# Kernel tuning notes

Hardware: AMD Instinct MI355X
Metric: run time of the kernel (lower is better)

The kernel has to match this reference:

```python
import jax, jax.numpy as jnp
import numpy as np

S, B, D, T = 256, 64, 1024, 64
BOS, EOS, PAD = 0, 1, 2


def setup_inputs() -> dict:
    key = jax.random.key(0)
    k1, k2, k3, k4, k5 = jax.random.split(key, 5)
    features = jax.random.normal(k1, (S, B, D), jnp.float32)
    tags = jax.random.randint(k2, (S, B), 0, T)
    # valid lengths in [2, S] so the recurrence and gold gather are well-defined
    seq_lens = jax.random.randint(k3, (B,), 2, S + 1)
    W = jax.random.normal(k4, (T, D), jnp.float32) * 0.02  # feat2tag weight
    b = jnp.zeros((T,), jnp.float32)                        # feat2tag bias
    transitions = jax.random.normal(k5, (T, T), jnp.float32) * 0.01
    return {"features": features, "tags": tags, "seq_lens": seq_lens,
            "W": W, "b": b, "transitions": transitions}


def reference(features, tags, seq_lens, W, b, transitions):
    s_len, b_size = features.shape[0], features.shape[1]
    n_tags = transitions.shape[0]
    # crf_scores[t, b, i, j] = emit[t, b, i] + transitions[i, j]
    emit = jnp.einsum('sbd,td->sbt', features, W) + b        # (S,B,T)
    crf = emit[:, :, :, None] + transitions[None, None]      # (S,B,T,T)

    # ---- gold path score ----
    pad_row = jnp.full((1, b_size), PAD, tags.dtype)
    nxt_tags = jnp.concatenate([tags[1:], pad_row], axis=0)  # (S,B)
    flat_ix = tags * n_tags + nxt_tags                       # (S,B)
    step_sc = jnp.take_along_axis(
        crf.reshape(s_len, b_size, n_tags * n_tags),
        flat_ix[:, :, None], axis=2)[..., 0]                 # (S,B)
    cum = jnp.cumsum(step_sc, axis=0)                        # (S,B)
    gold = cum[seq_lens - 1, jnp.arange(b_size)].sum()

    # ---- partition function via masked forward recurrence (scan over time) ----
    cur0 = crf[0, :, BOS, :]                                 # (B,T)
    active = jnp.arange(1, s_len)[:, None] < seq_lens[None, :]  # (S-1,B)

    def step(cur, xs):
        crf_t, act = xs                                      # (B,T,T), (B,)
        # logsumexp over previous tag i: cur[b,i] + crf_t[b,i,j]
        nxt = jax.nn.logsumexp(cur[:, :, None] + crf_t, axis=1)  # (B,T)
        return jnp.where(act[:, None], nxt, cur), None

    cur, _ = jax.lax.scan(step, cur0, (crf[1:], active))
    return cur[:, EOS].sum() - gold
```

## Files before the change

### kernel.cpp

```cpp
#include <hip/hip_runtime.h>

#define SLEN 256
#define NB   64
#define ND   1024
#define NT   64
#define APAD 1032

typedef float f32x4  __attribute__((ext_vector_type(4)));
typedef short bf16x8 __attribute__((ext_vector_type(8)));
typedef __fp16 f16x8 __attribute__((ext_vector_type(8)));
typedef __fp16 f16x2 __attribute__((ext_vector_type(2)));
typedef unsigned int u32;
typedef u32 u32x2 __attribute__((ext_vector_type(2)));
typedef u32 u32x4 __attribute__((ext_vector_type(4)));
typedef int  i32x4 __attribute__((ext_vector_type(4)));

__device__ __forceinline__ u32 cvt_pk_bf16(float lo, float hi) {
  u32 r;
  asm("v_cvt_pk_bf16_f32 %0, %1, %2" : "=v"(r) : "v"(lo), "v"(hi));
  return r;
}

__device__ __forceinline__ u32 cvt_pk_f16(float lo, float hi) {
  union { f16x2 h; u32 u; } c;
  c.h = __builtin_amdgcn_cvt_pkrtz(lo, hi);
  return c.u;
}

__device__ __forceinline__ u32 pack_f16_rne(float lo, float hi) {
  union { _Float16 h[2]; u32 u; } c;
  c.h[0] = (_Float16)lo;
  c.h[1] = (_Float16)hi;
  return c.u;
}

__device__ __forceinline__ unsigned short f2bf(float f) {
  u32 u = __float_as_uint(f);
  return (unsigned short)((u + 0x7FFFu + ((u >> 16) & 1u)) >> 16);
}

__device__ __forceinline__ f32x4 vmax4(f32x4 a, f32x4 b) {
  f32x4 r;
  r.x = fmaxf(a.x, b.x); r.y = fmaxf(a.y, b.y);
  r.z = fmaxf(a.z, b.z); r.w = fmaxf(a.w, b.w);
  return r;
}

__global__ __launch_bounds__(256) void prep(const float* __restrict__ W,
                                            const float* __restrict__ trans,
                                            unsigned short* __restrict__ Wb3,
                                            u32* __restrict__ Ebuf,
                                            float* __restrict__ out) {
  if (blockIdx.x < 256) {
    int o  = blockIdx.x * 256 + threadIdx.x;
    int e  = o & 7;
    int l  = (o >> 3) & 63;
    int f  = (o >> 9) & 3;
    int k0 = o >> 11;
    int t  = f * 16 + (l & 15);
    int k  = k0 * 32 + ((l >> 4) << 3) + e;
    Wb3[o] = f2bf(W[t * ND + k]);
    return;
  }
  const int tid = threadIdx.x;
  if (tid == 0) out[0] = 0.f;
  const int l = tid & 63, wd = tid >> 6;
  const int q = l >> 4, c = l & 15;
#pragma unroll
  for (int mt = 0; mt < 4; ++mt)
#pragma unroll
    for (int kf = 0; kf < 2; ++kf) {
      float v0 = __expf(trans[(32 * kf + 8 * q + 2 * wd)     * NT + 16 * mt + c]) * 0.015625f;
      float v1 = __expf(trans[(32 * kf + 8 * q + 2 * wd + 1) * NT + 16 * mt + c]) * 0.015625f;
      Ebuf[(mt * 2 + kf) * 256 + l * 4 + wd] = pack_f16_rne(v0, v1);
    }
}

__global__ __launch_bounds__(256) void emit_gemm(const float* __restrict__ F,
                                                 const unsigned short* __restrict__ Wb3,
                                                 const float* __restrict__ bias,
                                                 unsigned short* __restrict__ xbuf) {
  __shared__ union ShU {
    unsigned short a[16 * APAD];
    float comb[4][64][17];
  } sh;
  const int tid = threadIdx.x;
  const int w   = tid >> 6;
  const int l   = tid & 63;
  const int q   = l >> 4;
  const int c   = l & 15;

  const int blk = blockIdx.x;
  const float* fb = F + (size_t)blk * 16 * ND;

#pragma unroll 8
  for (int i = 0; i < 16; ++i) {
    f32x4 v = *(const f32x4*)(fb + i * ND + tid * 4);
    u32x2 p;
    p.x = cvt_pk_bf16(v.x, v.y);
    p.y = cvt_pk_bf16(v.z, v.w);
    *(u32x2*)(sh.a + i * APAD + tid * 4) = p;
  }
  __syncthreads();

  f32x4 acc0 = {0.f, 0.f, 0.f, 0.f};
  f32x4 acc1 = acc0, acc2 = acc0, acc3 = acc0;
  const bf16x8* bptr = reinterpret_cast<const bf16x8*>(Wb3) + l;
  const unsigned short* arow = sh.a + c * APAD + q * 8;

#pragma unroll
  for (int g = 0; g < 8; ++g) {
    int ks = w * 8 + g;
    bf16x8 af = *(const bf16x8*)(arow + ks * 32);
    bf16x8 b0 = bptr[(ks * 4 + 0) * 64];
    bf16x8 b1 = bptr[(ks * 4 + 1) * 64];
    bf16x8 b2 = bptr[(ks * 4 + 2) * 64];
    bf16x8 b3 = bptr[(ks * 4 + 3) * 64];
    acc0 = __builtin_amdgcn_mfma_f32_16x16x32_bf16(af, b0, acc0, 0, 0, 0);
    acc1 = __builtin_amdgcn_mfma_f32_16x16x32_bf16(af, b1, acc1, 0, 0, 0);
    acc2 = __builtin_amdgcn_mfma_f32_16x16x32_bf16(af, b2, acc2, 0, 0, 0);
    acc3 = __builtin_amdgcn_mfma_f32_16x16x32_bf16(af, b3, acc3, 0, 0, 0);
  }

  __syncthreads();
#pragma unroll
  for (int r = 0; r < 4; ++r) {
    sh.comb[w][l][r]      = acc0[r];
    sh.comb[w][l][4 + r]  = acc1[r];
    sh.comb[w][l][8 + r]  = acc2[r];
    sh.comb[w][l][12 + r] = acc3[r];
  }
  __syncthreads();

  {
    float s[4];
#pragma unroll
    for (int r = 0; r < 4; ++r)
      s[r] = sh.comb[0][l][4 * w + r] + sh.comb[1][l][4 * w + r]
           + sh.comb[2][l][4 * w + r] + sh.comb[3][l][4 * w + r];
    const float bv = bias[16 * w + c];
    unsigned short* op = xbuf + (size_t)(blk * 16 + q * 4) * NT + 16 * w + c;
#pragma unroll
    for (int r = 0; r < 4; ++r)
      op[r * NT] = f2bf(__expf(s[r] + bv));
  }
}

__global__ __launch_bounds__(256, 2) void chunk_prod(
    const unsigned short* __restrict__ xbuf, const float* __restrict__ trans,
    const u32* __restrict__ Ebuf, const int* __restrict__ tags,
    const int* __restrict__ seq_lens, unsigned short* __restrict__ Gout,
    int* __restrict__ Gscale, float* __restrict__ Gpart) {
  __shared__ float trs[64 * 68];
  __shared__ unsigned short xlds[34 * 64];
  const int b   = blockIdx.x >> 3;
  const int k   = blockIdx.x & 7;
  const int tid = threadIdx.x;
  const int wid = tid >> 6;
  const int l   = tid & 63;
  const int q   = l >> 4, c = l & 15;

  const int L = seq_lens[b];

  {
    int tp  = tid >> 3;
    int cg  = (tid & 7) * 8;
    const u32x4* s4 = (const u32x4*)(xbuf + ((size_t)((32 * k + tp) * NB + b)) * NT + cg);
    *(u32x4*)(xlds + tp * 64 + cg) = *s4;
  }

  if (wid == 0) {
    float gp = 0.f;
    int s = 32 * k + (l & 31);
    if (l < 32 && s < L) {
      int tg = tags[s * NB + b];
      int nx = (s + 1 < SLEN) ? tags[(s + 1) * NB + b] : 2;
      float xv = __uint_as_float((u32)xbuf[(size_t)(s * NB + b) * NT + tg] << 16);
      gp = __logf(xv) + trans[tg * NT + nx];
    }
    gp += __shfl_xor(gp, 1, 64);
    gp += __shfl_xor(gp, 2, 64);
    gp += __shfl_xor(gp, 4, 64);
    gp += __shfl_xor(gp, 8, 64);
    gp += __shfl_xor(gp, 16, 64);
    if (l == 0) Gpart[b * 8 + k] = gp;
  }

  union uf { u32x4 u; f16x8 v; };
  uf ef[4][2];
#pragma unroll
  for (int mt = 0; mt < 4; ++mt)
#pragma unroll
    for (int kf = 0; kf < 2; ++kf)
      ef[mt][kf].u = *(const u32x4*)(Ebuf + (mt * 2 + kf) * 256 + l * 4);

  f32x4 g0 = {0,0,0,0}, g1 = g0, g2 = g0, g3 = g0;
  {
    int r = c - 4 * q;
    if (r >= 0 && r < 4) {
      float one = 1.0f;
      if (wid == 0) g0[r & 3] = one;
      else if (wid == 1) g1[r & 3] = one;
      else if (wid == 2) g2[r & 3] = one;
      else g3[r & 3] = one;
    }
  }

  int tbeg = 32 * k; if (tbeg < 1) tbeg = 1;
  int tend = 32 * k + 32; if (tend > L) tend = L;
  int exw = 0;

  __syncthreads();

#define SWAPQ(A, B) do {                                                  \
    asm("v_permlane32_swap_b32 %0, %1" : "+v"(A), "+v"(B));               \
    asm("v_permlane16_swap_b32 %0, %1" : "+v"(A), "+v"(B));               \
  } while (0)

#define LOADX(X, TP) do {                                                 \
    X[0] = *(const u32x2*)(xlds + (TP) * 64 + 4 * q);                     \
    X[1] = *(const u32x2*)(xlds + (TP) * 64 + 16 + 4 * q);                \
    X[2] = *(const u32x2*)(xlds + (TP) * 64 + 32 + 4 * q);                \
    X[3] = *(const u32x2*)(xlds + (TP) * 64 + 48 + 4 * q);                \
  } while (0)

#define MULPK(P0, P1, G, XW) do {                                         \
    f32x4 xv;                                                             \
    xv.x = __uint_as_float(XW.x << 16);                                   \
    xv.y = __uint_as_float(XW.x & 0xFFFF0000u);                           \
    xv.z = __uint_as_float(XW.y << 16);                                   \
    xv.w = __uint_as_float(XW.y & 0xFFFF0000u);                           \
    f32x4 ww = G * xv;                                                    \
    P0 = cvt_pk_f16(ww.x, ww.y);                                          \
    P1 = cvt_pk_f16(ww.z, ww.w);                                          \
  } while (0)

#define STEPF(X, T) do {                                                  \
    if ((((T) & 7) == 0) && ((T) != tbeg)) {         \
      f32x4 m4 = vmax4(vmax4(g0, g1), vmax4(g2, g3));                     \
      float mx = fmaxf(fmaxf(m4.x, m4.y), fmaxf(m4.z, m4.w));             \
      mx = fmaxf(mx, __shfl_xor(mx, 1, 64));                              \
      mx = fmaxf(mx, __shfl_xor(mx, 2, 64));                              \
      mx = fmaxf(mx, __shfl_xor(mx, 4, 64));                              \
      mx = fmaxf(mx, __shfl_xor(mx, 8, 64));                              \
      mx = fmaxf(mx, __shfl_xor(mx, 16, 64));                             \
      mx = fmaxf(mx, __shfl_xor(mx, 32, 64));                             \
      int ex = (int)((__float_as_uint(mx) >> 23) & 255u) - 127;           \
      float sc = __uint_as_float((u32)(127 - ex) << 23);                  \
      g0 *= sc; g1 *= sc; g2 *= sc; g3 *= sc; exw += ex;                  \
    }                                                                     \
    u32 p00, p01, p10, p11, p20, p21, p30, p31;                           \
    MULPK(p00, p01, g0, X[0]);                                            \
    MULPK(p10, p11, g1, X[1]);                                            \
    MULPK(p20, p21, g2, X[2]);                                            \
    MULPK(p30, p31, g3, X[3]);                                            \
    SWAPQ(p00, p10); SWAPQ(p01, p11); SWAPQ(p20, p30); SWAPQ(p21, p31);   \
    uf B0, B1;                                                            \
    B0.u[0] = p00; B0.u[1] = p01; B0.u[2] = p10; B0.u[3] = p11;           \
    B1.u[0] = p20; B1.u[1] = p21; B1.u[2] = p30; B1.u[3] = p31;           \
    const f32x4 zz = {0.f, 0.f, 0.f, 0.f};                                \
    g0 = __builtin_amdgcn_mfma_f32_16x16x32_f16(ef[0][0].v, B0.v, zz, 0, 0, 0); \
    g0 = __builtin_amdgcn_mfma_f32_16x16x32_f16(ef[0][1].v, B1.v, g0, 0, 0, 0); \
    g1 = __builtin_amdgcn_mfma_f32_16x16x32_f16(ef[1][0].v, B0.v, zz, 0, 0, 0); \
    g1 = __builtin_amdgcn_mfma_f32_16x16x32_f16(ef[1][1].v, B1.v, g1, 0, 0, 0); \
    g2 = __builtin_amdgcn_mfma_f32_16x16x32_f16(ef[2][0].v, B0.v, zz, 0, 0, 0); \
    g2 = __builtin_amdgcn_mfma_f32_16x16x32_f16(ef[2][1].v, B1.v, g2, 0, 0, 0); \
    g3 = __builtin_amdgcn_mfma_f32_16x16x32_f16(ef[3][0].v, B0.v, zz, 0, 0, 0); \
    g3 = __builtin_amdgcn_mfma_f32_16x16x32_f16(ef[3][1].v, B1.v, g3, 0, 0, 0); \
  } while (0)

  if (tbeg < tend) {
    u32x2 XA[4], XB[4];
    int tp  = tbeg - 32 * k;
    int tpe = tend - 32 * k;
    LOADX(XA, tp);
    for (; tp + 1 < tpe; tp += 2) {
      LOADX(XB, tp + 1);
      STEPF(XA, tp + 32 * k);
      LOADX(XA, tp + 2);
      STEPF(XB, tp + 1 + 32 * k);
    }
    if (tp < tpe) STEPF(XA, tp + 32 * k);
  }
#undef STEPF
#undef MULPK
#undef LOADX
#undef SWAPQ

  if (l == 0) Gscale[((size_t)b * 8 + k) * 4 + wid] = exw;

#pragma unroll
  for (int r = 0; r < 4; ++r) {
    trs[(4 * q + r) * 68      + 16 * wid + c] = g0[r];
    trs[(16 + 4 * q + r) * 68 + 16 * wid + c] = g1[r];
    trs[(32 + 4 * q + r) * 68 + 16 * wid + c] = g2[r];
    trs[(48 + 4 * q + r) * 68 + 16 * wid + c] = g3[r];
  }
  __syncthreads();
  {
    int row = tid >> 2, qt = tid & 3;
    const float* src = trs + row * 68 + qt * 16;
    u32 wp[8];
#pragma unroll
    for (int m = 0; m < 8; ++m) wp[m] = cvt_pk_bf16(src[2 * m], src[2 * m + 1]);
    u32x4* dst = (u32x4*)(Gout + (((size_t)(b * 8 + k) * 64 + row) * 64 + qt * 16));
    dst[0] = *(u32x4*)&wp[0];
    dst[1] = *(u32x4*)&wp[4];
  }
}

__global__ __launch_bounds__(64, 1) void chain_apply(
    const unsigned short* __restrict__ xbuf, const float* __restrict__ trans,
    const unsigned short* __restrict__ Gout, const int* __restrict__ Gscale,
    const float* __restrict__ Gpart, const int* __restrict__ seq_lens,
    float* __restrict__ out) {
  __shared__ __align__(16) float elds[64];
  const int b = blockIdx.x;
  const int j = threadIdx.x;
  const int L = seq_lens[b];

  float gp = (j < 8) ? Gpart[b * 8 + j] : 0.f;
  gp += __shfl_xor(gp, 1, 64);
  gp += __shfl_xor(gp, 2, 64);
  gp += __shfl_xor(gp, 4, 64);

  float A    = __expf(trans[j]);
  float logZ = __logf(__uint_as_float((u32)xbuf[(size_t)b * NT] << 16));

  const unsigned short* gbase = Gout + (size_t)b * 8 * 4096 + (size_t)j * 64;
  const i32x4* sbase = (const i32x4*)(Gscale + (size_t)b * 8 * 4);
  u32x4 gc[8], gn[8];
  i32x4 scc, scn;
#pragma unroll
  for (int m = 0; m < 8; ++m) gc[m] = *((const u32x4*)gbase + m);
  scc = sbase[0];

  const float C6 = 6.f * 0.6931471805599453f;

  for (int k = 0; k < 8; ++k) {
    if (k < 7) {
      const u32x4* gb2 = (const u32x4*)(gbase + (size_t)(k + 1) * 4096);
#pragma unroll
      for (int m = 0; m < 8; ++m) gn[m] = gb2[m];
      scn = sbase[k + 1];
    }
    int tb = 32 * k; if (tb < 1) tb = 1;
    int te = 32 * k + 32; if (te > L) te = L;
    int n = te - tb;
    if (n > 0) {
      elds[j] = A;
      float sA0 = 0.f, sA1 = 0.f, sA2 = 0.f, sA3 = 0.f;
      float sB0 = 0.f, sB1 = 0.f, sB2 = 0.f, sB3 = 0.f;
#pragma unroll
      for (int m = 0; m < 8; ++m) {
        f32x4 av0 = *(const f32x4*)(elds + 8 * m);
        f32x4 av1 = *(const f32x4*)(elds + 8 * m + 4);
        u32x4 w = gc[m];
        float a0, a1;
        a0 = fmaf(av0.x, __uint_as_float(w.x << 16),         0.f);
        a0 = fmaf(av0.y, __uint_as_float(w.x & 0xFFFF0000u), a0);
        a0 = fmaf(av0.z, __uint_as_float(w.y << 16),         a0);
        a0 = fmaf(av0.w, __uint_as_float(w.y & 0xFFFF0000u), a0);
        a1 = fmaf(av1.x, __uint_as_float(w.z << 16),         0.f);
        a1 = fmaf(av1.y, __uint_as_float(w.z & 0xFFFF0000u), a1);
        a1 = fmaf(av1.z, __uint_as_float(w.w << 16),         a1);
        a1 = fmaf(av1.w, __uint_as_float(w.w & 0xFFFF0000u), a1);
        switch (m >> 1) {
          case 0: if (m & 1) { sB0 += a0 + a1; } else { sA0 += a0 + a1; } break;
          case 1: if (m & 1) { sB1 += a0 + a1; } else { sA1 += a0 + a1; } break;
          case 2: if (m & 1) { sB2 += a0 + a1; } else { sA2 += a0 + a1; } break;
          default: if (m & 1) { sB3 += a0 + a1; } else { sA3 += a0 + a1; } break;
        }
      }
      float sc0 = __uint_as_float((u32)(127 + scc.x) << 23);
      float sc1 = __uint_as_float((u32)(127 + scc.y) << 23);
      float sc2 = __uint_as_float((u32)(127 + scc.z) << 23);
      float sc3 = __uint_as_float((u32)(127 + scc.w) << 23);
      A = ((sA0 + sB0) * sc0 + (sA1 + sB1) * sc1)
        + ((sA2 + sB2) * sc2 + (sA3 + sB3) * sc3);
      logZ += C6 * (float)n;
      u32 bb = __builtin_amdgcn_readfirstlane(__float_as_uint(A));
      int ex = (int)((bb >> 23) & 255u) - 127;
      A *= __uint_as_float((u32)(127 - ex) << 23);
      logZ += (float)ex * 0.6931471805599453f;
    }
    if (k < 7) {
#pragma unroll
      for (int m = 0; m < 8; ++m) gc[m] = gn[m];
      scc = scn;
    }
  }

  float res = logZ + __logf(A);
  res = __shfl(res, 1, 64);
  if (j == 0) atomicAdd(out, res - gp);
}

extern "C" void kernel_launch(void* const* d_in, const int* in_sizes, int n_in,
                              void* d_out, int out_size, void* d_ws, size_t ws_size,
                              hipStream_t stream) {
  const float* F     = (const float*)d_in[0];
  const int*   tags  = (const int*)  d_in[1];
  const int*   seq   = (const int*)  d_in[2];
  const float* W     = (const float*)d_in[3];
  const float* bias  = (const float*)d_in[4];
  const float* trans = (const float*)d_in[5];
  float* out = (float*)d_out;

  char* ws = (char*)d_ws;
  unsigned short* xbuf   = (unsigned short*)ws;
  unsigned short* Wb3    = (unsigned short*)(ws + 2228224);
  u32*            Ebuf   = (u32*)(ws + 2359296);
  unsigned short* Gout   = (unsigned short*)(ws + 2367488);
  int*            Gscale = (int*)(ws + 6561792);
  float*          Gpart  = (float*)(ws + 6569984);

  prep       <<<257,  256, 0, stream>>>(W, trans, Wb3, Ebuf, out);
  emit_gemm  <<<1024, 256, 0, stream>>>(F, Wb3, bias, xbuf);
  chunk_prod <<<512,  256, 0, stream>>>(xbuf, trans, Ebuf, tags, seq, Gout, Gscale, Gpart);
  chain_apply<<<64,    64, 0, stream>>>(xbuf, trans, Gout, Gscale, Gpart, seq, out);
}
```

Before: 45.70 us.

## Switch chunk products to split bf16 MFMA with 16-step chunks, drop rescaling

Replaces the f16 transition-matrix MFMA with a hi/lo bf16 split (two bf16 MFMAs per product, summed), which removes the periodic in-chunk max/rescale reduction and the per-chunk exponent array. Chunks shrink from 32 to 16 time steps, doubling the chunk_prod grid and raising the occupancy hint. In return the sequential chain_apply must apply 16 chunk matrices instead of 8, and the per-step MFMA count doubles. The loop is also simplified to a single step per iteration without software prefetch of the next step's LDS data.

After: 52.65 us. +15.2%, slower.

```diff
diff --git a/kernel.cpp b/kernel.cpp
--- a/kernel.cpp
+++ b/kernel.cpp
@@ -8,12 +8,9 @@
 
 typedef float f32x4  __attribute__((ext_vector_type(4)));
 typedef short bf16x8 __attribute__((ext_vector_type(8)));
-typedef __fp16 f16x8 __attribute__((ext_vector_type(8)));
-typedef __fp16 f16x2 __attribute__((ext_vector_type(2)));
 typedef unsigned int u32;
 typedef u32 u32x2 __attribute__((ext_vector_type(2)));
 typedef u32 u32x4 __attribute__((ext_vector_type(4)));
-typedef int  i32x4 __attribute__((ext_vector_type(4)));
 
 __device__ __forceinline__ u32 cvt_pk_bf16(float lo, float hi) {
   u32 r;
@@ -21,29 +18,9 @@
   return r;
 }
 
-__device__ __forceinline__ u32 cvt_pk_f16(float lo, float hi) {
-  union { f16x2 h; u32 u; } c;
-  c.h = __builtin_amdgcn_cvt_pkrtz(lo, hi);
-  return c.u;
-}
-
-__device__ __forceinline__ u32 pack_f16_rne(float lo, float hi) {
-  union { _Float16 h[2]; u32 u; } c;
-  c.h[0] = (_Float16)lo;
-  c.h[1] = (_Float16)hi;
-  return c.u;
-}
-
 __device__ __forceinline__ unsigned short f2bf(float f) {
   u32 u = __float_as_uint(f);
   return (unsigned short)((u + 0x7FFFu + ((u >> 16) & 1u)) >> 16);
-}
-
-__device__ __forceinline__ f32x4 vmax4(f32x4 a, f32x4 b) {
-  f32x4 r;
-  r.x = fmaxf(a.x, b.x); r.y = fmaxf(a.y, b.y);
-  r.z = fmaxf(a.z, b.z); r.w = fmaxf(a.w, b.w);
-  return r;
 }
 
 __global__ __launch_bounds__(256) void prep(const float* __restrict__ W,
@@ -72,7 +49,11 @@
     for (int kf = 0; kf < 2; ++kf) {
       float v0 = __expf(trans[(32 * kf + 8 * q + 2 * wd)     * NT + 16 * mt + c]) * 0.015625f;
       float v1 = __expf(trans[(32 * kf + 8 * q + 2 * wd + 1) * NT + 16 * mt + c]) * 0.015625f;
-      Ebuf[(mt * 2 + kf) * 256 + l * 4 + wd] = pack_f16_rne(v0, v1);
+      u32 u0 = __float_as_uint(v0), u1 = __float_as_uint(v1);
+      float h0 = __uint_as_float((u0 + 0x7FFFu + ((u0 >> 16) & 1u)) & 0xFFFF0000u);
+      float h1 = __uint_as_float((u1 + 0x7FFFu + ((u1 >> 16) & 1u)) & 0xFFFF0000u);
+      Ebuf[((mt * 2 + kf) * 2 + 0) * 256 + l * 4 + wd] = cvt_pk_bf16(h0, h1);
+      Ebuf[((mt * 2 + kf) * 2 + 1) * 256 + l * 4 + wd] = cvt_pk_bf16(v0 - h0, v1 - h1);
     }
 }
 
@@ -146,15 +127,15 @@
   }
 }
 
-__global__ __launch_bounds__(256, 2) void chunk_prod(
+__global__ __launch_bounds__(256, 4) void chunk_prod(
     const unsigned short* __restrict__ xbuf, const float* __restrict__ trans,
     const u32* __restrict__ Ebuf, const int* __restrict__ tags,
     const int* __restrict__ seq_lens, unsigned short* __restrict__ Gout,
-    int* __restrict__ Gscale, float* __restrict__ Gpart) {
+    float* __restrict__ Gpart) {
   __shared__ float trs[64 * 68];
-  __shared__ unsigned short xlds[34 * 64];
-  const int b   = blockIdx.x >> 3;
-  const int k   = blockIdx.x & 7;
+  __shared__ unsigned short xlds[16 * 64];
+  const int b   = blockIdx.x >> 4;
+  const int k   = blockIdx.x & 15;
   const int tid = threadIdx.x;
   const int wid = tid >> 6;
   const int l   = tid & 63;
@@ -162,17 +143,17 @@
 
   const int L = seq_lens[b];
 
-  {
+  if (tid < 128) {
     int tp  = tid >> 3;
     int cg  = (tid & 7) * 8;
-    const u32x4* s4 = (const u32x4*)(xbuf + ((size_t)((32 * k + tp) * NB + b)) * NT + cg);
+    const u32x4* s4 = (const u32x4*)(xbuf + ((size_t)((16 * k + tp) * NB + b)) * NT + cg);
     *(u32x4*)(xlds + tp * 64 + cg) = *s4;
   }
 
   if (wid == 0) {
     float gp = 0.f;
-    int s = 32 * k + (l & 31);
-    if (l < 32 && s < L) {
+    int s = 16 * k + (l & 15);
+    if (l < 16 && s < L) {
       int tg = tags[s * NB + b];
       int nx = (s + 1 < SLEN) ? tags[(s + 1) * NB + b] : 2;
       float xv = __uint_as_float((u32)xbuf[(size_t)(s * NB + b) * NT + tg] << 16);
@@ -182,17 +163,18 @@
     gp += __shfl_xor(gp, 2, 64);
     gp += __shfl_xor(gp, 4, 64);
     gp += __shfl_xor(gp, 8, 64);
-    gp += __shfl_xor(gp, 16, 64);
-    if (l == 0) Gpart[b * 8 + k] = gp;
-  }
-
-  union uf { u32x4 u; f16x8 v; };
-  uf ef[4][2];
+    if (l == 0) Gpart[b * 16 + k] = gp;
+  }
+
+  union uf { u32x4 u; bf16x8 v; };
+  uf eh[4][2], el[4][2];
 #pragma unroll
   for (int mt = 0; mt < 4; ++mt)
 #pragma unroll
-    for (int kf = 0; kf < 2; ++kf)
-      ef[mt][kf].u = *(const u32x4*)(Ebuf + (mt * 2 + kf) * 256 + l * 4);
+    for (int kf = 0; kf < 2; ++kf) {
+      eh[mt][kf].u = *(const u32x4*)(Ebuf + ((mt * 2 + kf) * 2 + 0) * 256 + l * 4);
+      el[mt][kf].u = *(const u32x4*)(Ebuf + ((mt * 2 + kf) * 2 + 1) * 256 + l * 4);
+    }
 
   f32x4 g0 = {0,0,0,0}, g1 = g0, g2 = g0, g3 = g0;
   {
@@ -206,9 +188,8 @@
     }
   }
 
-  int tbeg = 32 * k; if (tbeg < 1) tbeg = 1;
-  int tend = 32 * k + 32; if (tend > L) tend = L;
-  int exw = 0;
+  int tbeg = 16 * k; if (tbeg < 1) tbeg = 1;
+  int tend = 16 * k + 16; if (tend > L) tend = L;
 
   __syncthreads();
 
@@ -231,24 +212,11 @@
     xv.z = __uint_as_float(XW.y << 16);                                   \
     xv.w = __uint_as_float(XW.y & 0xFFFF0000u);                           \
     f32x4 ww = G * xv;                                                    \
-    P0 = cvt_pk_f16(ww.x, ww.y);                                          \
-    P1 = cvt_pk_f16(ww.z, ww.w);                                          \
+    P0 = cvt_pk_bf16(ww.x, ww.y);                                         \
+    P1 = cvt_pk_bf16(ww.z, ww.w);                                         \
   } while (0)
 
-#define STEPF(X, T) do {                                                  \
-    if ((((T) & 7) == 0) && ((T) != tbeg)) {         \
-      f32x4 m4 = vmax4(vmax4(g0, g1), vmax4(g2, g3));                     \
-      float mx = fmaxf(fmaxf(m4.x, m4.y), fmaxf(m4.z, m4.w));             \
-      mx = fmaxf(mx, __shfl_xor(mx, 1, 64));                              \
-      mx = fmaxf(mx, __shfl_xor(mx, 2, 64));                              \
-      mx = fmaxf(mx, __shfl_xor(mx, 4, 64));                              \
-      mx = fmaxf(mx, __shfl_xor(mx, 8, 64));                              \
-      mx = fmaxf(mx, __shfl_xor(mx, 16, 64));                             \
-      mx = fmaxf(mx, __shfl_xor(mx, 32, 64));                             \
-      int ex = (int)((__float_as_uint(mx) >> 23) & 255u) - 127;           \
-      float sc = __uint_as_float((u32)(127 - ex) << 23);                  \
-      g0 *= sc; g1 *= sc; g2 *= sc; g3 *= sc; exw += ex;                  \
-    }                                                                     \
+#define STEPF(X) do {                                                     \
     u32 p00, p01, p10, p11, p20, p21, p30, p31;                           \
     MULPK(p00, p01, g0, X[0]);                                            \
     MULPK(p10, p11, g1, X[1]);                                            \
@@ -259,35 +227,38 @@
     B0.u[0] = p00; B0.u[1] = p01; B0.u[2] = p10; B0.u[3] = p11;           \
     B1.u[0] = p20; B1.u[1] = p21; B1.u[2] = p30; B1.u[3] = p31;           \
     const f32x4 zz = {0.f, 0.f, 0.f, 0.f};                                \
-    g0 = __builtin_amdgcn_mfma_f32_16x16x32_f16(ef[0][0].v, B0.v, zz, 0, 0, 0); \
-    g0 = __builtin_amdgcn_mfma_f32_16x16x32_f16(ef[0][1].v, B1.v, g0, 0, 0, 0); \
-    g1 = __builtin_amdgcn_mfma_f32_16x16x32_f16(ef[1][0].v, B0.v, zz, 0, 0, 0); \
-    g1 = __builtin_amdgcn_mfma_f32_16x16x32_f16(ef[1][1].v, B1.v, g1, 0, 0, 0); \
-    g2 = __builtin_amdgcn_mfma_f32_16x16x32_f16(ef[2][0].v, B0.v, zz, 0, 0, 0); \
-    g2 = __builtin_amdgcn_mfma_f32_16x16x32_f16(ef[2][1].v, B1.v, g2, 0, 0, 0); \
-    g3 = __builtin_amdgcn_mfma_f32_16x16x32_f16(ef[3][0].v, B0.v, zz, 0, 0, 0); \
-    g3 = __builtin_amdgcn_mfma_f32_16x16x32_f16(ef[3][1].v, B1.v, g3, 0, 0, 0); \
+    f32x4 dh, dl;                                                         \
+    dh = __builtin_amdgcn_mfma_f32_16x16x32_bf16(eh[0][0].v, B0.v, zz, 0, 0, 0); \
+    dh = __builtin_amdgcn_mfma_f32_16x16x32_bf16(eh[0][1].v, B1.v, dh, 0, 0, 0); \
+    dl = __builtin_amdgcn_mfma_f32_16x16x32_bf16(el[0][0].v, B0.v, zz, 0, 0, 0); \
+    dl = __builtin_amdgcn_mfma_f32_16x16x32_bf16(el[0][1].v, B1.v, dl, 0, 0, 0); \
+    g0 = dh + dl;                                                         \
+    dh = __builtin_amdgcn_mfma_f32_16x16x32_bf16(eh[1][0].v, B0.v, zz, 0, 0, 0); \
+    dh = __builtin_amdgcn_mfma_f32_16x16x32_bf16(eh[1][1].v, B1.v, dh, 0, 0, 0); \
+    dl = __builtin_amdgcn_mfma_f32_16x16x32_bf16(el[1][0].v, B0.v, zz, 0, 0, 0); \
+    dl = __builtin_amdgcn_mfma_f32_16x16x32_bf16(el[1][1].v, B1.v, dl, 0, 0, 0); \
+    g1 = dh + dl;                                                         \
+    dh = __builtin_amdgcn_mfma_f32_16x16x32_bf16(eh[2][0].v, B0.v, zz, 0, 0, 0); \
+    dh = __builtin_amdgcn_mfma_f32_16x16x32_bf16(eh[2][1].v, B1.v, dh, 0, 0, 0); \
+    dl = __builtin_amdgcn_mfma_f32_16x16x32_bf16(el[2][0].v, B0.v, zz, 0, 0, 0); \
+    dl = __builtin_amdgcn_mfma_f32_16x16x32_bf16(el[2][1].v, B1.v, dl, 0, 0, 0); \
+    g2 = dh + dl;                                                         \
+    dh = __builtin_amdgcn_mfma_f32_16x16x32_bf16(eh[3][0].v, B0.v, zz, 0, 0, 0); \
+    dh = __builtin_amdgcn_mfma_f32_16x16x32_bf16(eh[3][1].v, B1.v, dh, 0, 0, 0); \
+    dl = __builtin_amdgcn_mfma_f32_16x16x32_bf16(el[3][0].v, B0.v, zz, 0, 0, 0); \
+    dl = __builtin_amdgcn_mfma_f32_16x16x32_bf16(el[3][1].v, B1.v, dl, 0, 0, 0); \
+    g3 = dh + dl;                                                         \
   } while (0)
 
-  if (tbeg < tend) {
-    u32x2 XA[4], XB[4];
-    int tp  = tbeg - 32 * k;
-    int tpe = tend - 32 * k;
-    LOADX(XA, tp);
-    for (; tp + 1 < tpe; tp += 2) {
-      LOADX(XB, tp + 1);
-      STEPF(XA, tp + 32 * k);
-      LOADX(XA, tp + 2);
-      STEPF(XB, tp + 1 + 32 * k);
-    }
-    if (tp < tpe) STEPF(XA, tp + 32 * k);
+  for (int t = tbeg; t < tend; ++t) {
+    u32x2 X[4];
+    LOADX(X, t - 16 * k);
+    STEPF(X);
   }
 #undef STEPF
 #undef MULPK
 #undef LOADX
 #undef SWAPQ
-
-  if (l == 0) Gscale[((size_t)b * 8 + k) * 4 + wid] = exw;
 
 #pragma unroll
   for (int r = 0; r < 4; ++r) {
@@ -303,7 +274,7 @@
     u32 wp[8];
 #pragma unroll
     for (int m = 0; m < 8; ++m) wp[m] = cvt_pk_bf16(src[2 * m], src[2 * m + 1]);
-    u32x4* dst = (u32x4*)(Gout + (((size_t)(b * 8 + k) * 64 + row) * 64 + qt * 16));
+    u32x4* dst = (u32x4*)(Gout + (((size_t)(b * 16 + k) * 64 + row) * 64 + qt * 16));
     dst[0] = *(u32x4*)&wp[0];
     dst[1] = *(u32x4*)&wp[4];
   }
@@ -311,83 +282,65 @@
 
 __global__ __launch_bounds__(64, 1) void chain_apply(
     const unsigned short* __restrict__ xbuf, const float* __restrict__ trans,
-    const unsigned short* __restrict__ Gout, const int* __restrict__ Gscale,
-    const float* __restrict__ Gpart, const int* __restrict__ seq_lens,
-    float* __restrict__ out) {
+    const unsigned short* __restrict__ Gout, const float* __restrict__ Gpart,
+    const int* __restrict__ seq_lens, float* __restrict__ out) {
   __shared__ __align__(16) float elds[64];
   const int b = blockIdx.x;
   const int j = threadIdx.x;
   const int L = seq_lens[b];
 
-  float gp = (j < 8) ? Gpart[b * 8 + j] : 0.f;
+  float gp = (j < 16) ? Gpart[b * 16 + j] : 0.f;
   gp += __shfl_xor(gp, 1, 64);
   gp += __shfl_xor(gp, 2, 64);
   gp += __shfl_xor(gp, 4, 64);
+  gp += __shfl_xor(gp, 8, 64);
 
   float A    = __expf(trans[j]);
   float logZ = __logf(__uint_as_float((u32)xbuf[(size_t)b * NT] << 16));
 
-  const unsigned short* gbase = Gout + (size_t)b * 8 * 4096 + (size_t)j * 64;
-  const i32x4* sbase = (const i32x4*)(Gscale + (size_t)b * 8 * 4);
+  const unsigned short* gbase = Gout + (size_t)b * 16 * 4096 + (size_t)j * 64;
   u32x4 gc[8], gn[8];
-  i32x4 scc, scn;
 #pragma unroll
   for (int m = 0; m < 8; ++m) gc[m] = *((const u32x4*)gbase + m);
-  scc = sbase[0];
 
   const float C6 = 6.f * 0.6931471805599453f;
 
-  for (int k = 0; k < 8; ++k) {
-    if (k < 7) {
+  for (int k = 0; k < 16; ++k) {
+    if (k < 15) {
       const u32x4* gb2 = (const u32x4*)(gbase + (size_t)(k + 1) * 4096);
 #pragma unroll
       for (int m = 0; m < 8; ++m) gn[m] = gb2[m];
-      scn = sbase[k + 1];
-    }
-    int tb = 32 * k; if (tb < 1) tb = 1;
-    int te = 32 * k + 32; if (te > L) te = L;
+    }
+    int tb = 16 * k; if (tb < 1) tb = 1;
+    int te = 16 * k + 16; if (te > L) te = L;
     int n = te - tb;
     if (n > 0) {
       elds[j] = A;
-      float sA0 = 0.f, sA1 = 0.f, sA2 = 0.f, sA3 = 0.f;
-      float sB0 = 0.f, sB1 = 0.f, sB2 = 0.f, sB3 = 0.f;
+      float s0 = 0.f, s1 = 0.f, s2 = 0.f, s3 = 0.f;
 #pragma unroll
       for (int m = 0; m < 8; ++m) {
         f32x4 av0 = *(const f32x4*)(elds + 8 * m);
         f32x4 av1 = *(const f32x4*)(elds + 8 * m + 4);
         u32x4 w = gc[m];
-        float a0, a1;
-        a0 = fmaf(av0.x, __uint_as_float(w.x << 16),         0.f);
-        a0 = fmaf(av0.y, __uint_as_float(w.x & 0xFFFF0000u), a0);
-        a0 = fmaf(av0.z, __uint_as_float(w.y << 16),         a0);
-        a0 = fmaf(av0.w, __uint_as_float(w.y & 0xFFFF0000u), a0);
-        a1 = fmaf(av1.x, __uint_as_float(w.z << 16),         0.f);
-        a1 = fmaf(av1.y, __uint_as_float(w.z & 0xFFFF0000u), a1);
-        a1 = fmaf(av1.z, __uint_as_float(w.w << 16),         a1);
-        a1 = fmaf(av1.w, __uint_as_float(w.w & 0xFFFF0000u), a1);
-        switch (m >> 1) {
-          case 0: if (m & 1) { sB0 += a0 + a1; } else { sA0 += a0 + a1; } break;
-          case 1: if (m & 1) { sB1 += a0 + a1; } else { sA1 += a0 + a1; } break;
-          case 2: if (m & 1) { sB2 += a0 + a1; } else { sA2 += a0 + a1; } break;
-          default: if (m & 1) { sB3 += a0 + a1; } else { sA3 += a0 + a1; } break;
-        }
+        s0 = fmaf(av0.x, __uint_as_float(w.x << 16),         s0);
+        s1 = fmaf(av0.y, __uint_as_float(w.x & 0xFFFF0000u), s1);
+        s2 = fmaf(av0.z, __uint_as_float(w.y << 16),         s2);
+        s3 = fmaf(av0.w, __uint_as_float(w.y & 0xFFFF0000u), s3);
+        s0 = fmaf(av1.x, __uint_as_float(w.z << 16),         s0);
+        s1 = fmaf(av1.y, __uint_as_float(w.z & 0xFFFF0000u), s1);
+        s2 = fmaf(av1.z, __uint_as_float(w.w << 16),         s2);
+        s3 = fmaf(av1.w, __uint_as_float(w.w & 0xFFFF0000u), s3);
       }
-      float sc0 = __uint_as_float((u32)(127 + scc.x) << 23);
-      float sc1 = __uint_as_float((u32)(127 + scc.y) << 23);
-      float sc2 = __uint_as_float((u32)(127 + scc.z) << 23);
-      float sc3 = __uint_as_float((u32)(127 + scc.w) << 23);
-      A = ((sA0 + sB0) * sc0 + (sA1 + sB1) * sc1)
-        + ((sA2 + sB2) * sc2 + (sA3 + sB3) * sc3);
+      A = (s0 + s1) + (s2 + s3);
       logZ += C6 * (float)n;
       u32 bb = __builtin_amdgcn_readfirstlane(__float_as_uint(A));
       int ex = (int)((bb >> 23) & 255u) - 127;
       A *= __uint_as_float((u32)(127 - ex) << 23);
       logZ += (float)ex * 0.6931471805599453f;
     }
-    if (k < 7) {
+    if (k < 15) {
 #pragma unroll
       for (int m = 0; m < 8; ++m) gc[m] = gn[m];
-      scc = scn;
     }
   }
 
@@ -408,15 +361,14 @@
   float* out = (float*)d_out;
 
   char* ws = (char*)d_ws;
-  unsigned short* xbuf   = (unsigned short*)ws;
-  unsigned short* Wb3    = (unsigned short*)(ws + 2228224);
-  u32*            Ebuf   = (u32*)(ws + 2359296);
-  unsigned short* Gout   = (unsigned short*)(ws + 2367488);
-  int*            Gscale = (int*)(ws + 6561792);
-  float*          Gpart  = (float*)(ws + 6569984);
+  unsigned short* xbuf  = (unsigned short*)ws;
+  unsigned short* Wb3   = (unsigned short*)(ws + 2228224);
+  u32*            Ebuf  = (u32*)(ws + 2359296);
+  unsigned short* Gout  = (unsigned short*)(ws + 2375680);
+  float*          Gpart = (float*)(ws + 10764288);
 
   prep       <<<257,  256, 0, stream>>>(W, trans, Wb3, Ebuf, out);
   emit_gemm  <<<1024, 256, 0, stream>>>(F, Wb3, bias, xbuf);
-  chunk_prod <<<512,  256, 0, stream>>>(xbuf, trans, Ebuf, tags, seq, Gout, Gscale, Gpart);
-  chain_apply<<<64,    64, 0, stream>>>(xbuf, trans, Gout, Gscale, Gpart, seq, out);
-}
+  chunk_prod <<<1024, 256, 0, stream>>>(xbuf, trans, Ebuf, tags, seq, Gout, Gpart);
+  chain_apply<<<64,    64, 0, stream>>>(xbuf, trans, Gout, Gpart, seq, out);
+}
```
